# Performance work log

Measured on AMD Instinct MI355X. Metric: run time of the kernel, lower is better.

The kernel has to match this reference:

```python
import jax, jax.numpy as jnp
import numpy as np

E = 256       # embed_size
H2 = 2 * E    # feature / encoder-output dim
B = 128
S = 512
OUT = 256


def setup_inputs() -> dict:
    key = jax.random.key(0)
    ks = jax.random.split(key, 20)
    p = lambda k, shp: (jax.random.normal(k, shp, jnp.float32) * 0.05)
    return {
        "inputs": jax.random.normal(ks[0], (B, S, H2), jnp.float32),
        # encoder BiLSTM (input 2E, hidden E), pytorch gate order i,f,g,o
        "enc_Wih_f": p(ks[1], (4 * E, H2)), "enc_Whh_f": p(ks[2], (4 * E, E)),
        "enc_bih_f": p(ks[3], (4 * E,)),    "enc_bhh_f": p(ks[4], (4 * E,)),
        "enc_Wih_b": p(ks[5], (4 * E, H2)), "enc_Whh_b": p(ks[6], (4 * E, E)),
        "enc_bih_b": p(ks[7], (4 * E,)),    "enc_bhh_b": p(ks[8], (4 * E,)),
        # decoder LSTM (input 2E, hidden 2E); called with zero state each step,
        # so W_hh and the forget gate contribute exactly zero -> omitted.
        "dec_Wih": p(ks[9], (4 * H2, H2)),
        "dec_bih": p(ks[10], (4 * H2,)), "dec_bhh": p(ks[11], (4 * H2,)),
        # attention + output head
        "attW": p(ks[12], (H2, H2)), "attW_b": p(ks[13], (H2,)),
        "attU": p(ks[14], (1, H2)),  "attU_b": p(ks[15], (1,)),
        "outW": p(ks[16], (OUT, H2)), "outW_b": p(ks[17], (OUT,)),
    }


def _lstm_dir(x, Wih, Whh, bih, bhh, reverse):
    """Single-direction LSTM, zero init state. x: (B,S,D) -> (B,S,E)."""
    pre = jnp.einsum("bsd,gd->bsg", x, Wih) + bih + bhh  # (B,S,4E)
    Eh = Whh.shape[1]

    def step(carry, p):
        h, c = carry
        g = p + h @ Whh.T
        i, f, gg, o = jnp.split(g, 4, axis=-1)
        c = jax.nn.sigmoid(f) * c + jax.nn.sigmoid(i) * jnp.tanh(gg)
        h = jax.nn.sigmoid(o) * jnp.tanh(c)
        return (h, c), h

    bsz = x.shape[0]
    init = (jnp.zeros((bsz, Eh), x.dtype), jnp.zeros((bsz, Eh), x.dtype))
    _, hs = jax.lax.scan(step, init, jnp.swapaxes(pre, 0, 1), reverse=reverse)
    return jnp.swapaxes(hs, 0, 1)


def _dec_cell(x, Wih, bih, bhh):
    """One LSTM step with zero (h,c): forget term and h@Whh vanish."""
    g = x @ Wih.T + bih + bhh
    i, _f, gg, o = jnp.split(g, 4, axis=-1)
    c = jax.nn.sigmoid(i) * jnp.tanh(gg)
    return jax.nn.sigmoid(o) * jnp.tanh(c)


def reference(inputs, enc_Wih_f, enc_Whh_f, enc_bih_f, enc_bhh_f,
              enc_Wih_b, enc_Whh_b, enc_bih_b, enc_bhh_b,
              dec_Wih, dec_bih, dec_bhh,
              attW, attW_b, attU, attU_b, outW, outW_b):
    bsz, seq, _ = inputs.shape
    # BiLSTM encoder
    hf = _lstm_dir(inputs, enc_Wih_f, enc_Whh_f, enc_bih_f, enc_bhh_f, False)
    hb = _lstm_dir(inputs, enc_Wih_b, enc_Whh_b, enc_bih_b, enc_bhh_b, True)
    enc = jnp.concatenate([hf, hb], axis=-1)  # (B,S,2E)

    # per-step decoder: each torch call re-zeros the LSTM state; input chains
    x0 = enc[:, -1, :]  # (B,2E)

    def dstep(h, _):
        h = _dec_cell(h, dec_Wih, dec_bih, dec_bhh)
        return h, h

    _, dec_ys = jax.lax.scan(dstep, x0, None, length=seq)
    dec_out = jnp.swapaxes(dec_ys, 0, 1)  # (B,S,2E)

    ae_loss = jnp.mean((inputs - jax.lax.stop_gradient(dec_out)) ** 2)

    # attention pooling (softmax over size-1 axis -> all-ones, as in original)
    enc2 = inputs + enc
    att = jnp.tanh(enc2 @ attW.T + attW_b)
    w = jax.nn.softmax(att @ attU.T + attU_b, axis=2)      # (B,S,1)
    pooled = jnp.einsum("bsd,bso->bod", enc2, w)           # (B,1,2E)
    outputs = pooled @ outW.T + outW_b                      # (B,1,OUT)
    return outputs.reshape(bsz, 1, 1, OUT), ae_loss
```

## Files before the change

### kernel.cpp

```cpp
#include <hip/hip_runtime.h>
#include <hip/hip_bf16.h>
#include <hip/hip_fp16.h>
#include <stdint.h>

#define B_ 128
#define S_ 512
#define E_ 256
#define H2_ 512
#define G_ 1024
#define DG_ 2048
#define M_ (B_*S_)

typedef float f32x4 __attribute__((ext_vector_type(4)));
typedef short s16x8 __attribute__((ext_vector_type(8)));
typedef _Float16 h16x2 __attribute__((ext_vector_type(2)));

__device__ __forceinline__ float sigm(float x){ return 1.f/(1.f+__expf(-x)); }
__device__ __forceinline__ float tanh_f(float x){ return 1.f - 2.f/(__expf(2.f*x)+1.f); }

__device__ __forceinline__ void gload_lds16(const void* g, void* l){
  __builtin_amdgcn_global_load_lds(
      (const __attribute__((address_space(1))) void*)g,
      (__attribute__((address_space(3))) void*)l,
      16, 0, 0);
}

__device__ __forceinline__ uint32_t enc_e4m3(float f){
  uint32_t u = __float_as_uint(f);
  uint32_t s = (u >> 24) & 0x80u;
  float af = fabsf(f);
  if (!(af > 0.f)) return s;
  if (af >= 448.f) return s | 0x7Eu;
  int ex = (int)((u >> 23) & 0xFF) - 127;
  uint32_t man = u & 0x7FFFFFu;
  int bexp = ex + 7;
  if (bexp <= 0){
    uint32_t qi = (uint32_t)rintf(af * 512.f);
    if (qi > 8u) qi = 8u;
    return s | qi;
  }
  uint32_t keep = man >> 20;
  uint32_t rest = man & 0xFFFFFu;
  const uint32_t half = 0x80000u;
  if (rest > half || (rest == half && (keep & 1u))) keep++;
  if (keep == 8u){ keep = 0u; bexp++; }
  if (bexp >= 16) return s | 0x7Eu;
  if (bexp == 15 && keep == 7u) keep = 6u;
  return s | ((uint32_t)bexp << 3) | keep;
}

__device__ __forceinline__ uint32_t f32_to_fp8_byte(float v){
#if __has_builtin(__builtin_amdgcn_cvt_pk_fp8_f32)
  int pk = __builtin_amdgcn_cvt_pk_fp8_f32(v, v, 0, false);
  return (uint32_t)pk & 0xFFu;
#else
  return enc_e4m3(v);
#endif
}

__device__ __forceinline__ float dot2_f16(uint32_t a, uint32_t b, float acc){
#if __has_builtin(__builtin_amdgcn_fdot2)
  return __builtin_amdgcn_fdot2(__builtin_bit_cast(h16x2,a), __builtin_bit_cast(h16x2,b), acc, false);
#else
  __half2 ah = __builtin_bit_cast(__half2, a), bh = __builtin_bit_cast(__half2, b);
  float2 af = __half22float2(ah), bf = __half22float2(bh);
  return fmaf(af.x, bf.x, fmaf(af.y, bf.y, acc));
#endif
}

__global__ __launch_bounds__(512) void k_prep_enc(
    const float* __restrict__ wf, const float* __restrict__ wb,
    const float* __restrict__ bihf, const float* __restrict__ bhhf,
    const float* __restrict__ bihb, const float* __restrict__ bhhb,
    ushort* __restrict__ Wenc, float* __restrict__ bsum){
  int n = blockIdx.x, d = threadIdx.x;
  const float* src = (n < G_) ? (wf + (size_t)n*H2_) : (wb + (size_t)(n-G_)*H2_);
  __hip_bfloat16 h = __float2bfloat16(src[d]);
  Wenc[(size_t)n*H2_ + d] = __builtin_bit_cast(ushort, h);
  if (d == 0) bsum[n] = (n < G_) ? (bihf[n] + bhhf[n]) : (bihb[n-G_] + bhhb[n-G_]);
}

__global__ __launch_bounds__(64) void k_prep_whh_pk(
    const float* __restrict__ whf, const float* __restrict__ whb, uint8_t* __restrict__ Wp){
  int bid = blockIdx.x;
  int lane = threadIdx.x;
  int d   = bid >> 8;
  int rem = bid & 255;
  int wid = rem >> 4;
  int gt  = (rem >> 2) & 3;
  int p   = rem & 3;
  const float* src = d ? whb : whf;
  int row = gt*256 + wid*16 + (lane & 15);
  int hk  = (lane >> 4) * 8;
  uint8_t bytes[16];
  #pragma unroll
  for (int e = 0; e < 8; ++e){
    bytes[e]     = (uint8_t)enc_e4m3(src[(size_t)row*E_ + (2*p)*32   + hk + e]);
    bytes[8 + e] = (uint8_t)enc_e4m3(src[(size_t)row*E_ + (2*p+1)*32 + hk + e]);
  }
  uint8_t* dst = Wp + ((size_t)bid)*1024 + lane*16;
  *(uint4*)dst = *(const uint4*)bytes;
}

__global__ __launch_bounds__(64) void k_prep_dec(
    const float* __restrict__ wd, const float* __restrict__ bih, const float* __restrict__ bhh,
    uint4* __restrict__ wdt, float* __restrict__ bsumd){
  int row = blockIdx.x, u = threadIdx.x;
  const float* src = wd + (size_t)row*H2_ + u*8;
  union { _Float16 h[8]; uint4 q; } pk;
  #pragma unroll
  for (int i=0;i<8;i++) pk.h[i] = (_Float16)src[i];
  wdt[(size_t)u*DG_ + row] = pk.q;
  if (u == 0) bsumd[row] = bih[row] + bhh[row];
}

__global__ __launch_bounds__(512) void k_xstat(
    const float* __restrict__ X, float* __restrict__ SX, float* __restrict__ SX2){
  int b = blockIdx.x, d = threadIdx.x;
  const float* xb = X + (size_t)b*S_*H2_;
  float s=0.f, s2=0.f;
  for (int t=0;t<S_;++t){ float v = xb[(size_t)t*H2_ + d]; s += v; s2 = fmaf(v,v,s2); }
  SX[(size_t)b*H2_+d]=s; SX2[(size_t)b*H2_+d]=s2;
}

__global__ __launch_bounds__(256) void k_gemm_pre_t(
    const float* __restrict__ X, const ushort* __restrict__ Wenc,
    const float* __restrict__ bsum, ushort* __restrict__ preT){
  __shared__ __align__(16) ushort smem[128*130];
  ushort (*As)[64] = (ushort (*)[64])(smem);
  ushort (*Bs)[64] = (ushort (*)[64])(smem + 8192);
  int n0 = blockIdx.x * 128;
  int tt = blockIdx.y;
  int tid = threadIdx.x, lane = tid & 63, wq = tid >> 6;
  int wr = wq >> 1, wc = wq & 1;
  f32x4 acc[4][4] = {};
  for (int kt=0; kt<8; ++kt){
    int k0 = kt*64;
    #pragma unroll
    for (int it=0; it<4; ++it){
      int slot = tid + it*256;
      int r = slot >> 3, c8 = (slot & 7)*8;
      const float* ap = X + ((size_t)(r*512 + tt))*512 + k0 + c8;
      float4 a0 = *(const float4*)ap;
      float4 a1 = *(const float4*)(ap+4);
      union { __hip_bfloat16 h[8]; uint4 q; } pk;
      pk.h[0]=__float2bfloat16(a0.x); pk.h[1]=__float2bfloat16(a0.y);
      pk.h[2]=__float2bfloat16(a0.z); pk.h[3]=__float2bfloat16(a0.w);
      pk.h[4]=__float2bfloat16(a1.x); pk.h[5]=__float2bfloat16(a1.y);
      pk.h[6]=__float2bfloat16(a1.z); pk.h[7]=__float2bfloat16(a1.w);
      *(uint4*)&As[r][c8] = pk.q;
      *(uint4*)&Bs[r][c8] = *(const uint4*)(Wenc + (size_t)(n0+r)*512 + k0 + c8);
    }
    __syncthreads();
    #pragma unroll
    for (int kk=0; kk<2; ++kk){
      int krow = kk*32 + (lane>>4)*8;
      s16x8 af[4], bf[4];
      #pragma unroll
      for (int mi=0;mi<4;mi++) af[mi] = *(const s16x8*)&As[wr*64+mi*16+(lane&15)][krow];
      #pragma unroll
      for (int ni=0;ni<4;ni++) bf[ni] = *(const s16x8*)&Bs[wc*64+ni*16+(lane&15)][krow];
      #pragma unroll
      for (int mi=0;mi<4;mi++){
        #pragma unroll
        for (int ni=0;ni<4;ni++)
          acc[mi][ni] = __builtin_amdgcn_mfma_f32_16x16x32_bf16(af[mi], bf[ni], acc[mi][ni], 0,0,0);
      }
    }
    __syncthreads();
  }
  #pragma unroll
  for (int ni=0; ni<4; ++ni){
    int n_l = wc*64 + ni*16 + (lane&15);
    float bs = bsum[n0 + n_l];
    #pragma unroll
    for (int mi=0; mi<4; ++mi){
      int bb = wr*64 + mi*16 + (lane>>4)*4;
      #pragma unroll
      for (int r2=0;r2<4;r2++){
        __hip_bfloat16 hv = __float2bfloat16(acc[mi][ni][r2] + bs);
        smem[n_l*130 + bb + r2] = __builtin_bit_cast(ushort, hv);
      }
    }
  }
  __syncthreads();
  #pragma unroll
  for (int it=0; it<64; ++it){
    int n_l = it*2 + (tid>>7);
    int b = tid & 127;
    preT[(((size_t)tt*8 + (b>>4))*2048 + n0 + n_l)*16 + (b & 15)] = smem[n_l*130 + b];
  }
}

__global__ __launch_bounds__(1024) void k_enc_mfma(
    const ushort* __restrict__ preT, const uint8_t* __restrict__ Wp,
    float* __restrict__ SH, float* __restrict__ x0){
  int wg = blockIdx.x;
  int dir = wg >> 3;
  int b0q = wg & 7;
  int b0 = b0q * 16;
  int t = threadIdx.x, lane = t & 63, wid = t >> 6;
  __shared__ __align__(16) uint4  wlds[16*7*64];
  __shared__ __align__(16) ushort pbuf[2048*8];
  __shared__ __align__(16) uint8_t hb[2][16*264];

  const uint4* wp0 = (const uint4*)(Wp + ((size_t)(dir*16 + wid))*16384);
  #pragma unroll
  for (int c=0; c<7; ++c)
    wlds[(wid*7 + c)*64 + lane] = wp0[c*64 + lane];
  for (int i=t; i<2*16*264; i+=1024) ((uint8_t*)hb)[i] = 0;

  int frow = lane & 15;
  int mb = (lane >> 4) * 4;
  int u0 = wid*16 + frow;
  float c_st[4] = {0,0,0,0};
  float sumh[4] = {0,0,0,0};
  __syncthreads();

  int pb = 0;
  for (int s=0; s<S_; ++s){
    int ts = dir ? (S_-1-s) : s;
    {
      const uint8_t* gb = (const uint8_t*)(preT + (((size_t)ts*8 + b0q)*2048 + (size_t)dir*1024)*16);
      uint8_t* lb = (uint8_t*)pbuf;
      #pragma unroll
      for (int c=0; c<2; ++c)
        gload_lds16(gb + (((wid*2 + c)*64 + lane) << 4), lb + (wid*2 + c)*1024);
    }
    long long a_ll[8];
    {
      const uint8_t* ar = &hb[pb][frow*264 + ((lane>>4)*8)];
      #pragma unroll
      for (int kk=0; kk<8; ++kk){
        uint2 v = *(const uint2*)(ar + kk*32);
        a_ll[kk] = (((long long)v.y) << 32) | (unsigned int)v.x;
      }
    }
    const uint4* wl = wp0;
    const uint4* wl2 = &wlds[(wid*7)*64 + lane];
    asm volatile("" : "+v"(wl), "+v"(wl2));
    f32x4 acc[4] = {};
    #pragma unroll
    for (int gt=0; gt<4; ++gt){
      #pragma unroll
      for (int p=0; p<4; ++p){
        int c = gt*4 + p;
        uint4 q = (c < 7) ? wl2[c*64] : wl[c*64 + lane];
        long long bf0 = (((long long)q.y) << 32) | (unsigned int)q.x;
        long long bf1 = (((long long)q.w) << 32) | (unsigned int)q.z;
        acc[gt] = __builtin_amdgcn_mfma_f32_16x16x32_fp8_fp8(a_ll[2*p],   bf0, acc[gt], 0,0,0);
        acc[gt] = __builtin_amdgcn_mfma_f32_16x16x32_fp8_fp8(a_ll[2*p+1], bf1, acc[gt], 0,0,0);
      }
    }
    __syncthreads();
    int wx0 = (dir==0 && s==S_-1) || (dir==1 && s==0);
    uint2 pvv[4];
    #pragma unroll
    for (int gt=0; gt<4; ++gt)
      pvv[gt] = *(const uint2*)&pbuf[(gt*256 + u0)*16 + mb];
    #pragma unroll
    for (int r=0; r<4; ++r){
      unsigned w0 = (r < 2) ? pvv[0].x : pvv[0].y;
      unsigned w1 = (r < 2) ? pvv[1].x : pvv[1].y;
      unsigned w2 = (r < 2) ? pvv[2].x : pvv[2].y;
      unsigned w3 = (r < 2) ? pvv[3].x : pvv[3].y;
      unsigned sh16 = (r & 1) ? 16u : 0u;
      float gi = acc[0][r] + __uint_as_float(((w0 >> sh16) & 0xFFFFu) << 16);
      float gf = acc[1][r] + __uint_as_float(((w1 >> sh16) & 0xFFFFu) << 16);
      float gg = acc[2][r] + __uint_as_float(((w2 >> sh16) & 0xFFFFu) << 16);
      float go = acc[3][r] + __uint_as_float(((w3 >> sh16) & 0xFFFFu) << 16);
      float cn = sigm(gf)*c_st[r] + sigm(gi)*tanh_f(gg);
      float hn = sigm(go)*tanh_f(cn);
      c_st[r] = cn;
      sumh[r] += hn;
      hb[pb^1][(mb+r)*264 + u0] = (uint8_t)f32_to_fp8_byte(hn);
      if (wx0) x0[(size_t)(b0+mb+r)*H2_ + dir*E_ + u0] = hn;
    }
    __syncthreads();
    pb ^= 1;
  }
  #pragma unroll
  for (int r=0; r<4; ++r)
    SH[((size_t)dir*B_ + b0 + mb + r)*E_ + u0] = sumh[r];
}

#define EPS_CONV 2e-6f
__global__ __launch_bounds__(512) void k_dec(
    const float* __restrict__ X, const uint4* __restrict__ wdt,
    const float* __restrict__ bsumd, const float* __restrict__ x0,
    const float* __restrict__ SX, const float* __restrict__ SX2,
    float* __restrict__ loss_b){
  int b = blockIdx.x, j = threadIdx.x;
  __shared__ _Float16 hl[512];
  __shared__ float red[512];
  float h = x0[(size_t)b*H2_ + j];
  hl[j] = (_Float16)h;
  float bi = bsumd[j], bg = bsumd[j+1024], bo = bsumd[j+1536];
  float sxp = 0.f, x2p = 0.f, lacc = 0.f;
  const float* xb = X + (size_t)b*S_*H2_;
  int done = S_;
  __syncthreads();
  for (int s=0; s<S_; ++s){
    float ai = bi, ag = bg, ao = bo;
    const uint4* hp = (const uint4*)hl;
    const uint4* wi = wdt + j;
    const uint4* wgp = wdt + j + 1024;
    const uint4* wo = wdt + j + 1536;
    #pragma unroll 8
    for (int u=0; u<64; ++u){
      uint4 hv = hp[u];
      uint4 a = wi[(size_t)u*DG_];
      uint4 g = wgp[(size_t)u*DG_];
      uint4 o = wo[(size_t)u*DG_];
      ai = dot2_f16(a.x, hv.x, ai); ai = dot2_f16(a.y, hv.y, ai);
      ai = dot2_f16(a.z, hv.z, ai); ai = dot2_f16(a.w, hv.w, ai);
      ag = dot2_f16(g.x, hv.x, ag); ag = dot2_f16(g.y, hv.y, ag);
      ag = dot2_f16(g.z, hv.z, ag); ag = dot2_f16(g.w, hv.w, ag);
      ao = dot2_f16(o.x, hv.x, ao); ao = dot2_f16(o.y, hv.y, ao);
      ao = dot2_f16(o.z, hv.z, ao); ao = dot2_f16(o.w, hv.w, ao);
    }
    float cc = sigm(ai) * tanh_f(ag);
    float hn = sigm(ao) * tanh_f(cc);
    float xv = xb[(size_t)s*H2_ + j];
    float dd = xv - hn;
    lacc += dd*dd; sxp += xv; x2p = fmaf(xv,xv,x2p);
    float delta = fabsf(hn - h);
    h = hn;
    __syncthreads();
    hl[j] = (_Float16)h;
    if (__syncthreads_count(delta > EPS_CONV) == 0){ done = s+1; break; }
  }
  if (done < S_){
    size_t o = (size_t)b*H2_ + j;
    float rx = SX[o] - sxp, rx2 = SX2[o] - x2p;
    float rem = (float)(S_ - done);
    lacc += rx2 - 2.f*h*rx + rem*h*h;
  }
  red[j] = lacc;
  __syncthreads();
  for (int st=256; st>0; st>>=1){
    if (j < st) red[j] += red[j+st];
    __syncthreads();
  }
  if (j == 0) loss_b[b] = red[0];
}

__global__ __launch_bounds__(256) void k_out(
    const float* __restrict__ SX, const float* __restrict__ SH,
    const float* __restrict__ outW, const float* __restrict__ outWb,
    const float* __restrict__ loss_b, float* __restrict__ out){
  int b = blockIdx.x, o = threadIdx.x;
  __shared__ float pooled[512];
  for (int d=o; d<512; d+=256){
    float v = SX[(size_t)b*H2_ + d];
    v += (d < E_) ? SH[(size_t)b*E_ + d] : SH[(size_t)(B_ + b)*E_ + (d - E_)];
    pooled[d] = v;
  }
  __syncthreads();
  const float4* w4 = (const float4*)(outW + (size_t)o*H2_);
  const float4* p4 = (const float4*)pooled;
  float acc = outWb[o];
  #pragma unroll 16
  for (int i=0;i<128;i++){
    float4 w = w4[i], p = p4[i];
    acc = fmaf(w.x,p.x,acc); acc = fmaf(w.y,p.y,acc);
    acc = fmaf(w.z,p.z,acc); acc = fmaf(w.w,p.w,acc);
  }
  out[(size_t)b*256 + o] = acc;
  if (b == 0 && o == 0){
    float L = 0.f;
    for (int i=0;i<B_;i++) L += loss_b[i];
    out[32768] = L / 33554432.f;
  }
}

extern "C" void kernel_launch(void* const* d_in, const int* in_sizes, int n_in,
                              void* d_out, int out_size, void* d_ws, size_t ws_size,
                              hipStream_t stream) {
  const float* X     = (const float*)d_in[0];
  const float* Wihf  = (const float*)d_in[1];
  const float* Whhf  = (const float*)d_in[2];
  const float* bihf  = (const float*)d_in[3];
  const float* bhhf  = (const float*)d_in[4];
  const float* Wihb  = (const float*)d_in[5];
  const float* Whhb  = (const float*)d_in[6];
  const float* bihb  = (const float*)d_in[7];
  const float* bhhb  = (const float*)d_in[8];
  const float* Wdec  = (const float*)d_in[9];
  const float* dbih  = (const float*)d_in[10];
  const float* dbhh  = (const float*)d_in[11];
  const float* outW  = (const float*)d_in[16];
  const float* outWb = (const float*)d_in[17];
  float* out = (float*)d_out;

  char* ws = (char*)d_ws;
  size_t off = 0;
  auto alloc = [&](size_t bytes){ void* p = ws + off; off += (bytes + 255) & ~(size_t)255; return p; };
  ushort* preT         = (ushort*)alloc((size_t)S_*DG_*B_*2);
  ushort* Wenc         = (ushort*)alloc((size_t)DG_*H2_*2);
  float* bsum          = (float*)alloc((size_t)DG_*4);
  uint8_t* Wp          = (uint8_t*)alloc((size_t)2*G_*E_);
  uint4* wdt           = (uint4*)alloc((size_t)64*DG_*16);
  float* bsumd         = (float*)alloc((size_t)DG_*4);
  float* SX            = (float*)alloc((size_t)B_*H2_*4);
  float* SX2           = (float*)alloc((size_t)B_*H2_*4);
  float* SH            = (float*)alloc((size_t)2*B_*E_*4);
  float* x0            = (float*)alloc((size_t)B_*H2_*4);
  float* loss_b        = (float*)alloc((size_t)B_*4);

  hipLaunchKernelGGL(k_prep_enc, dim3(DG_), dim3(512), 0, stream,
                     Wihf, Wihb, bihf, bhhf, bihb, bhhb, Wenc, bsum);
  hipLaunchKernelGGL(k_prep_whh_pk, dim3(512), dim3(64), 0, stream, Whhf, Whhb, Wp);
  hipLaunchKernelGGL(k_prep_dec, dim3(DG_), dim3(64), 0, stream, Wdec, dbih, dbhh, wdt, bsumd);
  hipLaunchKernelGGL(k_xstat, dim3(B_), dim3(H2_), 0, stream, X, SX, SX2);
  hipLaunchKernelGGL(k_gemm_pre_t, dim3(16, 512), dim3(256), 0, stream, X, Wenc, bsum, preT);
  hipLaunchKernelGGL(k_enc_mfma, dim3(16), dim3(1024), 0, stream, preT, Wp, SH, x0);
  hipLaunchKernelGGL(k_dec, dim3(B_), dim3(512), 0, stream, X, wdt, bsumd, x0, SX, SX2, loss_b);
  hipLaunchKernelGGL(k_out, dim3(B_), dim3(256), 0, stream, SX, SH, outW, outWb, loss_b, out);
}
```

Before: 3.423 ms.

## Store gate pre-activations in MFMA fragment layout and drop LDS staging

The GEMM epilogue now writes bf16 pre-activations straight from MFMA accumulators into a per-(step, batch-tile, dir, gate) plane layout that matches each thread's fragment. This removes the LDS transpose in the GEMM. The recurrent kernel then loads its four gate values directly into registers, so it no longer needs the global-to-LDS copy or one __syncthreads per step. The freed LDS lets more W_hh chunks sit in shared memory (9 instead of 7), and the remaining chunks are hoisted into registers before the MFMA loop. The costs are more register pressure and less coalesced 8-byte global stores in the GEMM.

```diff
diff --git a/kernel.cpp b/kernel.cpp
--- a/kernel.cpp
+++ b/kernel.cpp
@@ -17,13 +17,6 @@
 
 __device__ __forceinline__ float sigm(float x){ return 1.f/(1.f+__expf(-x)); }
 __device__ __forceinline__ float tanh_f(float x){ return 1.f - 2.f/(__expf(2.f*x)+1.f); }
-
-__device__ __forceinline__ void gload_lds16(const void* g, void* l){
-  __builtin_amdgcn_global_load_lds(
-      (const __attribute__((address_space(1))) void*)g,
-      (__attribute__((address_space(3))) void*)l,
-      16, 0, 0);
-}
 
 __device__ __forceinline__ uint32_t enc_e4m3(float f){
   uint32_t u = __float_as_uint(f);
@@ -125,10 +118,9 @@
 
 __global__ __launch_bounds__(256) void k_gemm_pre_t(
     const float* __restrict__ X, const ushort* __restrict__ Wenc,
-    const float* __restrict__ bsum, ushort* __restrict__ preT){
-  __shared__ __align__(16) ushort smem[128*130];
-  ushort (*As)[64] = (ushort (*)[64])(smem);
-  ushort (*Bs)[64] = (ushort (*)[64])(smem + 8192);
+    const float* __restrict__ bsum, uint8_t* __restrict__ preP){
+  __shared__ __align__(16) ushort As[128][64];
+  __shared__ __align__(16) ushort Bs[128][64];
   int n0 = blockIdx.x * 128;
   int tt = blockIdx.y;
   int tid = threadIdx.x, lane = tid & 63, wq = tid >> 6;
@@ -169,45 +161,43 @@
     }
     __syncthreads();
   }
+  int dir = n0 >> 10;
+  int gt  = (n0 & 1023) >> 8;
+  int nb2 = n0 & 255;
   #pragma unroll
   for (int ni=0; ni<4; ++ni){
     int n_l = wc*64 + ni*16 + (lane&15);
     float bs = bsum[n0 + n_l];
+    int tbase = ((nb2 + wc*64 + ni*16) >> 4) * 64;
     #pragma unroll
     for (int mi=0; mi<4; ++mi){
-      int bb = wr*64 + mi*16 + (lane>>4)*4;
+      union { ushort h[4]; uint2 q; } pk2;
       #pragma unroll
       for (int r2=0;r2<4;r2++){
         __hip_bfloat16 hv = __float2bfloat16(acc[mi][ni][r2] + bs);
-        smem[n_l*130 + bb + r2] = __builtin_bit_cast(ushort, hv);
+        pk2.h[r2] = __builtin_bit_cast(ushort, hv);
       }
-    }
-  }
-  __syncthreads();
-  #pragma unroll
-  for (int it=0; it<64; ++it){
-    int n_l = it*2 + (tid>>7);
-    int b = tid & 127;
-    preT[(((size_t)tt*8 + (b>>4))*2048 + n0 + n_l)*16 + (b & 15)] = smem[n_l*130 + b];
+      size_t plane = (((size_t)tt*8 + (wr*4+mi))*2 + dir)*4 + gt;
+      *(uint2*)(preP + plane*8192 + (size_t)(tbase + lane)*8) = pk2.q;
+    }
   }
 }
 
 __global__ __launch_bounds__(1024) void k_enc_mfma(
-    const ushort* __restrict__ preT, const uint8_t* __restrict__ Wp,
+    const uint8_t* __restrict__ preP, const uint8_t* __restrict__ Wp,
     float* __restrict__ SH, float* __restrict__ x0){
   int wg = blockIdx.x;
   int dir = wg >> 3;
   int b0q = wg & 7;
   int b0 = b0q * 16;
   int t = threadIdx.x, lane = t & 63, wid = t >> 6;
-  __shared__ __align__(16) uint4  wlds[16*7*64];
-  __shared__ __align__(16) ushort pbuf[2048*8];
+  __shared__ __align__(16) uint4  wlds[16*9*64];
   __shared__ __align__(16) uint8_t hb[2][16*264];
 
   const uint4* wp0 = (const uint4*)(Wp + ((size_t)(dir*16 + wid))*16384);
   #pragma unroll
-  for (int c=0; c<7; ++c)
-    wlds[(wid*7 + c)*64 + lane] = wp0[c*64 + lane];
+  for (int c=0; c<9; ++c)
+    wlds[(wid*9 + c)*64 + lane] = wp0[c*64 + lane];
   for (int i=t; i<2*16*264; i+=1024) ((uint8_t*)hb)[i] = 0;
 
   int frow = lane & 15;
@@ -220,13 +210,11 @@
   int pb = 0;
   for (int s=0; s<S_; ++s){
     int ts = dir ? (S_-1-s) : s;
-    {
-      const uint8_t* gb = (const uint8_t*)(preT + (((size_t)ts*8 + b0q)*2048 + (size_t)dir*1024)*16);
-      uint8_t* lb = (uint8_t*)pbuf;
-      #pragma unroll
-      for (int c=0; c<2; ++c)
-        gload_lds16(gb + (((wid*2 + c)*64 + lane) << 4), lb + (wid*2 + c)*1024);
-    }
+    const uint8_t* pp = preP + ((((size_t)ts*8 + b0q)*2 + dir)*4)*8192 + (size_t)t*8;
+    uint2 pg0 = *(const uint2*)pp;
+    uint2 pg1 = *(const uint2*)(pp + 8192);
+    uint2 pg2 = *(const uint2*)(pp + 16384);
+    uint2 pg3 = *(const uint2*)(pp + 24576);
     long long a_ll[8];
     {
       const uint8_t* ar = &hb[pb][frow*264 + ((lane>>4)*8)];
@@ -237,27 +225,26 @@
       }
     }
     const uint4* wl = wp0;
-    const uint4* wl2 = &wlds[(wid*7)*64 + lane];
+    const uint4* wl2 = &wlds[(wid*9)*64 + lane];
     asm volatile("" : "+v"(wl), "+v"(wl2));
+    uint4 qs[7];
+    #pragma unroll
+    for (int i=0; i<7; ++i) qs[i] = wl[(9+i)*64 + lane];
     f32x4 acc[4] = {};
     #pragma unroll
     for (int gt=0; gt<4; ++gt){
       #pragma unroll
       for (int p=0; p<4; ++p){
         int c = gt*4 + p;
-        uint4 q = (c < 7) ? wl2[c*64] : wl[c*64 + lane];
+        uint4 q = (c < 9) ? wl2[c*64] : qs[c-9];
         long long bf0 = (((long long)q.y) << 32) | (unsigned int)q.x;
         long long bf1 = (((long long)q.w) << 32) | (unsigned int)q.z;
         acc[gt] = __builtin_amdgcn_mfma_f32_16x16x32_fp8_fp8(a_ll[2*p],   bf0, acc[gt], 0,0,0);
         acc[gt] = __builtin_amdgcn_mfma_f32_16x16x32_fp8_fp8(a_ll[2*p+1], bf1, acc[gt], 0,0,0);
       }
     }
-    __syncthreads();
     int wx0 = (dir==0 && s==S_-1) || (dir==1 && s==0);
-    uint2 pvv[4];
-    #pragma unroll
-    for (int gt=0; gt<4; ++gt)
-      pvv[gt] = *(const uint2*)&pbuf[(gt*256 + u0)*16 + mb];
+    uint2 pvv[4] = {pg0, pg1, pg2, pg3};
     #pragma unroll
     for (int r=0; r<4; ++r){
       unsigned w0 = (r < 2) ? pvv[0].x : pvv[0].y;
@@ -396,7 +383,7 @@
   char* ws = (char*)d_ws;
   size_t off = 0;
   auto alloc = [&](size_t bytes){ void* p = ws + off; off += (bytes + 255) & ~(size_t)255; return p; };
-  ushort* preT         = (ushort*)alloc((size_t)S_*DG_*B_*2);
+  uint8_t* preP        = (uint8_t*)alloc((size_t)S_*8*2*4*8192);
   ushort* Wenc         = (ushort*)alloc((size_t)DG_*H2_*2);
   float* bsum          = (float*)alloc((size_t)DG_*4);
   uint8_t* Wp          = (uint8_t*)alloc((size_t)2*G_*E_);
@@ -413,8 +400,8 @@
   hipLaunchKernelGGL(k_prep_whh_pk, dim3(512), dim3(64), 0, stream, Whhf, Whhb, Wp);
   hipLaunchKernelGGL(k_prep_dec, dim3(DG_), dim3(64), 0, stream, Wdec, dbih, dbhh, wdt, bsumd);
   hipLaunchKernelGGL(k_xstat, dim3(B_), dim3(H2_), 0, stream, X, SX, SX2);
-  hipLaunchKernelGGL(k_gemm_pre_t, dim3(16, 512), dim3(256), 0, stream, X, Wenc, bsum, preT);
-  hipLaunchKernelGGL(k_enc_mfma, dim3(16), dim3(1024), 0, stream, preT, Wp, SH, x0);
+  hipLaunchKernelGGL(k_gemm_pre_t, dim3(16, 512), dim3(256), 0, stream, X, Wenc, bsum, preP);
+  hipLaunchKernelGGL(k_enc_mfma, dim3(16), dim3(1024), 0, stream, preP, Wp, SH, x0);
   hipLaunchKernelGGL(k_dec, dim3(B_), dim3(512), 0, stream, X, wdt, bsumd, x0, SX, SX2, loss_b);
   hipLaunchKernelGGL(k_out, dim3(B_), dim3(256), 0, stream, SX, SH, outW, outWb, loss_b, out);
 }
```

New measurement: 4.380 ms. 1.28x slower.
